# Optimization experiments

Measured on AMD Instinct MI355X. Metric: run time of the kernel, lower is better.

## Reference

```python
import jax, jax.numpy as jnp
import numpy as np

EMBED = 1024
HEADS = 16
HEAD_DIM = EMBED // HEADS
WIN = 256  # attention_window w; band width = 2w+1


def setup_inputs() -> dict:
    key = jax.random.key(0)
    ks = jax.random.split(key, 10)
    b, s, e = 2, 4096, EMBED
    scale = 1.0 / np.sqrt(e)
    inp = {"x": jax.random.normal(ks[0], (b, s, e), jnp.float32)}
    for i, (wn, bn) in enumerate([("Wq", "bq"), ("Wk", "bk"), ("Wv", "bv"), ("Wo", "bo")]):
        inp[wn] = jax.random.normal(ks[1 + i], (e, e), jnp.float32) * scale
        inp[bn] = jax.random.normal(ks[5 + i], (e,), jnp.float32) * 0.01
    return inp


def _rope_headaxis(x):
    # Replicates RotaryEmbedding applied to [b, s, h, d]: the original indexes
    # x.shape[2] (== num_heads here), so phase varies over the HEAD axis.
    h, d = x.shape[2], x.shape[3]
    inv = 1.0 / (10000.0 ** (jnp.arange(0, d, 2, dtype=jnp.float32) / d))
    freqs = jnp.arange(h, dtype=jnp.float32)[:, None] * inv[None, :]
    emb = jnp.concatenate([freqs, freqs], axis=-1)  # [h, d]
    cos = jnp.cos(emb)[None, None]  # [1,1,h,d]
    sin = jnp.sin(emb)[None, None]
    x2 = jnp.stack([-x[..., 1::2], x[..., 0::2]], axis=-1).reshape(x.shape)
    return x * cos + x2 * sin


def reference(x, Wq, bq, Wk, bk, Wv, bv, Wo, bo):
    b, s, e = x.shape
    h, d, w = HEADS, HEAD_DIM, WIN
    q = (x @ Wq.T + bq).reshape(b, s, h, d)
    k = (x @ Wk.T + bk).reshape(b, s, h, d)
    v = (x @ Wv.T + bv).reshape(b, s, h, d)
    q = _rope_headaxis(q) / jnp.sqrt(jnp.float32(d))
    k = _rope_headaxis(k)

    # Band (sliding-window) attention: query chunk c of size w attends to key
    # chunks c-1, c, c+1 (3w keys); relative-position + boundary masking makes
    # this identical to the original sliding_chunks band of width 2w+1.
    nc = s // w
    qc = q.reshape(b, nc, w, h, d)
    pad = [(0, 0), (w, w), (0, 0), (0, 0)]
    kp = jnp.pad(k, pad)
    vp = jnp.pad(v, pad)
    idx = jnp.arange(nc)[:, None] * w + jnp.arange(3 * w)[None, :]  # [nc, 3w]
    k3 = kp[:, idx]  # [b, nc, 3w, h, d]
    v3 = vp[:, idx]
    scores = jnp.einsum('bcxhd,bcyhd->bhcxy', qc, k3)  # [b,h,nc,w,3w]

    c = jnp.arange(nc)[:, None, None]
    xq = jnp.arange(w)[None, :, None]
    y = jnp.arange(3 * w)[None, None, :]
    kpos = c * w + y - w  # absolute key position
    valid = (y >= xq) & (y <= xq + 2 * w) & (kpos >= 0) & (kpos < s)
    scores = jnp.where(valid[None, None], scores, -jnp.inf)

    probs = jax.nn.softmax(scores, axis=-1)  # fp32 softmax, as in original
    ctx = jnp.einsum('bhcxy,bcyhd->bcxhd', probs, v3).reshape(b, s, e)
    return ctx @ Wo.T + bo
```

## Files before the change

### kernel.cpp

```cpp
#include <hip/hip_runtime.h>


typedef _Float16 half8 __attribute__((ext_vector_type(8)));
typedef _Float16 half4v __attribute__((ext_vector_type(4)));
typedef float floatx4 __attribute__((ext_vector_type(4)));

typedef __attribute__((address_space(3))) unsigned int lds_u32;
typedef const __attribute__((address_space(1))) unsigned int glb_u32;

__device__ __forceinline__ void async_copy16(const void* g, void* l) {
  __builtin_amdgcn_global_load_lds((glb_u32*)g, (lds_u32*)l, 16, 0, 0);
}

__global__ __launch_bounds__(256) void convert_kernel(
    const float* __restrict__ x, const float* __restrict__ wq,
    const float* __restrict__ wk, const float* __restrict__ wv,
    const float* __restrict__ wo, _Float16* __restrict__ dst) {
  const int e0 = (blockIdx.x * 256 + threadIdx.x) * 4;
  const float* src; int off;
  if      (e0 <  8388608) { src = x;  off = e0; }
  else if (e0 <  9437184) { src = wq; off = e0 -  8388608; }
  else if (e0 < 10485760) { src = wk; off = e0 -  9437184; }
  else if (e0 < 11534336) { src = wv; off = e0 - 10485760; }
  else                    { src = wo; off = e0 - 11534336; }
  const float4 f = *(const float4*)(src + off);
  half4v h;
  h[0] = (_Float16)f.x; h[1] = (_Float16)f.y;
  h[2] = (_Float16)f.z; h[3] = (_Float16)f.w;
  *(half4v*)(dst + e0) = h;
}

__global__ __launch_bounds__(256, 2) void gemm_qkv_kernel(
    const _Float16* __restrict__ A, const _Float16* __restrict__ w0,
    const _Float16* __restrict__ w1, const _Float16* __restrict__ w2,
    const float* __restrict__ b0, const float* __restrict__ b1,
    const float* __restrict__ b2, _Float16* __restrict__ o0,
    _Float16* __restrict__ o1, _Float16* __restrict__ o2) {
  __shared__ _Float16 smem[17408];
  _Float16* As = smem;
  _Float16* Bs = smem + 8192;

  const int tid = threadIdx.x;
  const int w = tid >> 6, lane = tid & 63;
  const int l4 = lane & 15, quad = lane >> 4;
  const int wm = w & 1, wn = w >> 1;

  const int bid = blockIdx.x;
  const int xcd = bid & 7, li = bid >> 3;
  const int z = li >> 6, r_ = li & 63;
  const int n_l = r_ >> 3, m_l = r_ & 7;
  const int m0 = (xcd * 8 + m_l) * 128;
  const int n0 = n_l * 128;

  const _Float16* B; const float* bias; _Float16* out;
  if (z == 0)      { B = w0; bias = b0; out = o0; }
  else if (z == 1) { B = w1; bias = b1; out = o1; }
  else             { B = w2; bias = b2; out = o2; }
  const bool dorope = z < 2;
  const float scl = (z == 0) ? 0.18033688f : 1.0f;

  const floatx4 zero = {0.f, 0.f, 0.f, 0.f};
  floatx4 acc[4][4];
#pragma unroll
  for (int i = 0; i < 4; ++i)
#pragma unroll
    for (int j = 0; j < 4; ++j) acc[i][j] = zero;

  for (int kt = 0; kt < 16; ++kt) {
    const int k0 = kt * 64;
#pragma unroll
    for (int i = 0; i < 4; ++i) {
      const int p = i * 256 + tid;
      const int r = p >> 3;
      const int c = (p & 7) ^ (r & 7);
      async_copy16(A + (m0 + r) * 1024 + k0 + c * 8, As + (i * 256 + w * 64) * 8);
      async_copy16(B + (n0 + r) * 1024 + k0 + c * 8, Bs + (i * 256 + w * 64) * 8);
    }
    __syncthreads();
#pragma unroll
    for (int ks = 0; ks < 2; ++ks) {
      half8 af[4], bf[4];
#pragma unroll
      for (int mt = 0; mt < 4; ++mt)
        af[mt] = *(const half8*)(As + (wm * 64 + mt * 16 + l4) * 64 +
                                 (((ks * 4 + quad) ^ (l4 & 7)) * 8));
#pragma unroll
      for (int nt = 0; nt < 4; ++nt)
        bf[nt] = *(const half8*)(Bs + (wn * 64 + nt * 16 + l4) * 64 +
                                 (((ks * 4 + quad) ^ (l4 & 7)) * 8));
#pragma unroll
      for (int mt = 0; mt < 4; ++mt)
#pragma unroll
        for (int nt = 0; nt < 4; ++nt)
          acc[mt][nt] = __builtin_amdgcn_mfma_f32_16x16x32_f16(af[mt], bf[nt], acc[mt][nt], 0, 0, 0);
    }
    __syncthreads();
  }

  _Float16* tile = smem;
#pragma unroll
  for (int nt = 0; nt < 4; ++nt) {
    const int n = n0 + wn * 64 + nt * 16 + l4;
    const float bval = bias[n];
    const int hh = n >> 6;
    float c_ = 1.f, ss = 0.f;
    if (dorope) {
      const float freq = __expf((float)(n & 31) * -0.28782314f);
      float s_;
      __sincosf((float)hh * freq, &s_, &c_);
      ss = (n & 1) ? s_ : -s_;
    }
#pragma unroll
    for (int mt = 0; mt < 4; ++mt)
#pragma unroll
      for (int r = 0; r < 4; ++r) {
        float val = acc[mt][nt][r] + bval;
        const float prt = __shfl_xor(val, 1);
        if (dorope) val = (val * c_ + prt * ss) * scl;
        tile[(wm * 64 + mt * 16 + quad * 4 + r) * 132 + wn * 64 + nt * 16 + l4] = (_Float16)val;
      }
  }
  __syncthreads();
#pragma unroll
  for (int j = 0; j < 8; ++j) {
    const int idx = j * 256 + tid;
    const int row = idx >> 4, cb = idx & 15;
    const int n = n0 + cb * 8;
    const int hh = n >> 6, dd = n & 63;
    const int m = m0 + row, bb = m >> 12, s = m & 4095;
    const half8 vals = *(const half8*)(tile + row * 132 + cb * 8);
    *(half8*)(out + ((bb * 16 + hh) * 4096 + s) * 64 + dd) = vals;
  }
}

__global__ __launch_bounds__(256, 2) void gemm_out_kernel(
    const _Float16* __restrict__ A, const _Float16* __restrict__ B,
    const float* __restrict__ bias, float* __restrict__ out) {
  __shared__ _Float16 smem[16384];
  _Float16* As = smem;
  _Float16* Bs = smem + 8192;

  const int tid = threadIdx.x;
  const int w = tid >> 6, lane = tid & 63;
  const int l4 = lane & 15, quad = lane >> 4;
  const int wm = w & 1, wn = w >> 1;

  const int bid = blockIdx.x;
  const int xcd = bid & 7, li = bid >> 3;
  const int n_l = li >> 3, m_l = li & 7;
  const int m0 = (xcd * 8 + m_l) * 128;
  const int n0 = n_l * 128;

  const floatx4 zero = {0.f, 0.f, 0.f, 0.f};
  floatx4 acc[4][4];
#pragma unroll
  for (int i = 0; i < 4; ++i)
#pragma unroll
    for (int j = 0; j < 4; ++j) acc[i][j] = zero;

  for (int kt = 0; kt < 16; ++kt) {
    const int k0 = kt * 64;
#pragma unroll
    for (int i = 0; i < 4; ++i) {
      const int p = i * 256 + tid;
      const int r = p >> 3;
      const int c = (p & 7) ^ (r & 7);
      async_copy16(A + (m0 + r) * 1024 + k0 + c * 8, As + (i * 256 + w * 64) * 8);
      async_copy16(B + (n0 + r) * 1024 + k0 + c * 8, Bs + (i * 256 + w * 64) * 8);
    }
    __syncthreads();
#pragma unroll
    for (int ks = 0; ks < 2; ++ks) {
      half8 af[4], bf[4];
#pragma unroll
      for (int mt = 0; mt < 4; ++mt)
        af[mt] = *(const half8*)(As + (wm * 64 + mt * 16 + l4) * 64 +
                                 (((ks * 4 + quad) ^ (l4 & 7)) * 8));
#pragma unroll
      for (int nt = 0; nt < 4; ++nt)
        bf[nt] = *(const half8*)(Bs + (wn * 64 + nt * 16 + l4) * 64 +
                                 (((ks * 4 + quad) ^ (l4 & 7)) * 8));
#pragma unroll
      for (int mt = 0; mt < 4; ++mt)
#pragma unroll
        for (int nt = 0; nt < 4; ++nt)
          acc[mt][nt] = __builtin_amdgcn_mfma_f32_16x16x32_f16(af[mt], bf[nt], acc[mt][nt], 0, 0, 0);
    }
    __syncthreads();
  }

#pragma unroll
  for (int nt = 0; nt < 4; ++nt) {
    const int n = n0 + wn * 64 + nt * 16 + l4;
    const float bval = bias[n];
#pragma unroll
    for (int mt = 0; mt < 4; ++mt)
#pragma unroll
      for (int r = 0; r < 4; ++r) {
        const int m = m0 + wm * 64 + mt * 16 + quad * 4 + r;
        out[m * 1024 + n] = acc[mt][nt][r] + bval;
      }
  }
}

__global__ __launch_bounds__(256) void transpose_v(const _Float16* __restrict__ v,
                                                   _Float16* __restrict__ vt) {
  __shared__ _Float16 tile[64 * 70];
  const int t = threadIdx.x;
  const int bh = blockIdx.y, s0 = blockIdx.x * 64;
  const _Float16* src = v + (bh * 4096 + s0) * 64;
#pragma unroll
  for (int i = 0; i < 2; ++i) {
    const int c = i * 256 + t;
    const int row = c >> 3, cb = c & 7;
    const half8 d = *(const half8*)(src + row * 64 + cb * 8);
#pragma unroll
    for (int u = 0; u < 8; ++u) tile[(cb * 8 + u) * 70 + row] = d[u];
  }
  __syncthreads();
  _Float16* dst = vt + bh * 262144 + s0;
#pragma unroll
  for (int i = 0; i < 2; ++i) {
    const int c = i * 256 + t;
    const int dd = c >> 3, scb = c & 7;
    half8 d;
#pragma unroll
    for (int u = 0; u < 8; ++u) d[u] = tile[dd * 70 + scb * 8 + u];
    *(half8*)(dst + dd * 4096 + scb * 8) = d;
  }
}

__global__ __launch_bounds__(256, 2) void attn_kernel(
    const _Float16* __restrict__ qg, const _Float16* __restrict__ kg,
    const _Float16* __restrict__ vtg, _Float16* __restrict__ ctx) {
  __shared__ _Float16 Ks[128 * 64];
  __shared__ _Float16 Vs[64 * 128];

  const int tid = threadIdx.x;
  const int w = tid >> 6, lane = tid & 63;
  const int l4 = lane & 15, quad = lane >> 4;
  const int q0 = blockIdx.x * 128;
  const int bh = blockIdx.y;
  const _Float16* qbh = qg + bh * 262144;
  const _Float16* kbh = kg + bh * 262144;
  const _Float16* vbh = vtg + bh * 262144;

  half8 qf[2][2];
#pragma unroll
  for (int nt = 0; nt < 2; ++nt)
#pragma unroll
    for (int ks = 0; ks < 2; ++ks)
      qf[nt][ks] = *(const half8*)(qbh + (q0 + w * 32 + nt * 16 + l4) * 64 + ks * 32 + quad * 8);

  const floatx4 zero = {0.f, 0.f, 0.f, 0.f};
  floatx4 OT[4][2];
  float m_st[2], l_st[2];
#pragma unroll
  for (int md = 0; md < 4; ++md)
#pragma unroll
    for (int nt = 0; nt < 2; ++nt) OT[md][nt] = zero;
#pragma unroll
  for (int nt = 0; nt < 2; ++nt) { m_st[nt] = -1e30f; l_st[nt] = 0.f; }

  for (int t = 0; t < 5; ++t) {
    const int kv0 = q0 + (t - 2) * 128;
    if (kv0 < 0 || kv0 >= 4096) continue;

#pragma unroll
    for (int i = 0; i < 4; ++i) {
      const int p = i * 256 + tid;
      const int rk = p >> 3, ck = (p & 7) ^ (rk & 7);
      async_copy16(kbh + (kv0 + rk) * 64 + ck * 8, Ks + (i * 256 + w * 64) * 8);
      const int rv = p >> 4, cv = (p & 15) ^ (rv & 7);
      async_copy16(vbh + rv * 4096 + kv0 + cv * 8, Vs + (i * 256 + w * 64) * 8);
    }
    __syncthreads();

    const bool edge = (t == 0 || t == 4);
#pragma unroll
    for (int hf = 0; hf < 2; ++hf) {
      const int kb = hf * 64;

      floatx4 ST[4][2];
#pragma unroll
      for (int m = 0; m < 4; ++m)
#pragma unroll
        for (int nt = 0; nt < 2; ++nt) ST[m][nt] = zero;
#pragma unroll
      for (int ks = 0; ks < 2; ++ks)
#pragma unroll
        for (int m = 0; m < 4; ++m) {
          const half8 kf = *(const half8*)(Ks + (kb + m * 16 + l4) * 64 +
                                           ((ks * 4 + quad) ^ (l4 & 7)) * 8);
#pragma unroll
          for (int nt = 0; nt < 2; ++nt)
            ST[m][nt] = __builtin_amdgcn_mfma_f32_16x16x32_f16(kf, qf[nt][ks], ST[m][nt], 0, 0, 0);
        }

      if (edge) {
#pragma unroll
        for (int m = 0; m < 4; ++m)
#pragma unroll
          for (int r = 0; r < 4; ++r) {
            const int key = kv0 + kb + m * 16 + quad * 4 + r;
#pragma unroll
            for (int nt = 0; nt < 2; ++nt) {
              const int d = key - (q0 + w * 32 + nt * 16 + l4);
              if (d < -256 || d > 256) ST[m][nt][r] = -1e30f;
            }
          }
      }

#pragma unroll
      for (int nt = 0; nt < 2; ++nt) {
        float mx = -1e30f;
#pragma unroll
        for (int m = 0; m < 4; ++m)
#pragma unroll
          for (int r = 0; r < 4; ++r) mx = fmaxf(mx, ST[m][nt][r]);
        mx = fmaxf(mx, __shfl_xor(mx, 16));
        mx = fmaxf(mx, __shfl_xor(mx, 32));
        const float mnew = fmaxf(m_st[nt], mx);
        const float alpha = exp2f(m_st[nt] - mnew);
        m_st[nt] = mnew;
        float rs = 0.f;
#pragma unroll
        for (int m = 0; m < 4; ++m)
#pragma unroll
          for (int r = 0; r < 4; ++r) {
            const float pv = exp2f(ST[m][nt][r] - mnew);
            ST[m][nt][r] = pv;
            rs += pv;
          }
        rs += __shfl_xor(rs, 16);
        rs += __shfl_xor(rs, 32);
        l_st[nt] = l_st[nt] * alpha + rs;
#pragma unroll
        for (int md = 0; md < 4; ++md)
#pragma unroll
          for (int r = 0; r < 4; ++r) OT[md][nt][r] *= alpha;
      }

#pragma unroll
      for (int m = 0; m < 4; ++m) {
        half4v pb[2];
#pragma unroll
        for (int nt = 0; nt < 2; ++nt) {
          const auto lo = __builtin_amdgcn_cvt_pkrtz(ST[m][nt][0], ST[m][nt][1]);
          const auto hi = __builtin_amdgcn_cvt_pkrtz(ST[m][nt][2], ST[m][nt][3]);
          pb[nt][0] = (_Float16)lo[0]; pb[nt][1] = (_Float16)lo[1];
          pb[nt][2] = (_Float16)hi[0]; pb[nt][3] = (_Float16)hi[1];
        }
#pragma unroll
        for (int md = 0; md < 4; ++md) {
          const half4v vf = *(const half4v*)(Vs + (md * 16 + l4) * 128 +
                                             (((hf * 8 + m * 2 + (quad >> 1)) ^ (l4 & 7)) * 8 +
                                              (quad & 1) * 4));
#pragma unroll
          for (int nt = 0; nt < 2; ++nt)
            OT[md][nt] = __builtin_amdgcn_mfma_f32_16x16x16f16(vf, pb[nt], OT[md][nt], 0, 0, 0);
        }
      }
    }
    __syncthreads();
  }

  const int b = bh >> 4, hh = bh & 15;
#pragma unroll
  for (int nt = 0; nt < 2; ++nt) {
    const float inv_l = 1.f / l_st[nt];
    const int s = q0 + w * 32 + nt * 16 + l4;
#pragma unroll
    for (int md = 0; md < 4; ++md) {
      half4v o;
#pragma unroll
      for (int r = 0; r < 4; ++r) o[r] = (_Float16)(OT[md][nt][r] * inv_l);
      *(half4v*)(ctx + (b * 4096 + s) * 1024 + hh * 64 + md * 16 + quad * 4) = o;
    }
  }
}

extern "C" void kernel_launch(void* const* d_in, const int* in_sizes, int n_in,
                              void* d_out, int out_size, void* d_ws, size_t ws_size,
                              hipStream_t stream) {
  const float* x  = (const float*)d_in[0];
  const float* Wq = (const float*)d_in[1];
  const float* bq = (const float*)d_in[2];
  const float* Wk = (const float*)d_in[3];
  const float* bk = (const float*)d_in[4];
  const float* Wv = (const float*)d_in[5];
  const float* bv = (const float*)d_in[6];
  const float* Wo = (const float*)d_in[7];
  const float* bo = (const float*)d_in[8];

  _Float16* ws   = (_Float16*)d_ws;
  _Float16* xh   = ws;
  _Float16* wqh  = ws + 8388608;
  _Float16* wkh  = ws + 9437184;
  _Float16* wvh  = ws + 10485760;
  _Float16* woh  = ws + 11534336;
  _Float16* qh   = ws + 12582912;
  _Float16* kh   = ws + 20971520;
  _Float16* vh   = ws + 29360128;
  _Float16* vth  = ws + 37748736;
  _Float16* ctxh = xh;

  convert_kernel<<<12288, 256, 0, stream>>>(x, Wq, Wk, Wv, Wo, ws);
  gemm_qkv_kernel<<<1536, 256, 0, stream>>>(xh, wqh, wkh, wvh,
                                            bq, bk, bv, qh, kh, vh);
  transpose_v<<<dim3(64, 32), 256, 0, stream>>>(vh, vth);
  attn_kernel<<<dim3(32, 32), 256, 0, stream>>>(qh, kh, vth, ctxh);
  gemm_out_kernel<<<512, 256, 0, stream>>>(ctxh, woh, bo, (float*)d_out);
}
```

Before: 256.6 us.

## Fuse V transpose into QKV GEMM epilogue and raise occupancy bounds

The QKV GEMM epilogue now writes the V projection directly in transposed [d, s] layout by staging through LDS transposed, removing the separate transpose_v kernel and its extra global read/write pass. Launch bounds for the GEMM and attention kernels are raised from 2 to 4 blocks per CU to raise occupancy. The occupancy hint tightens the register budget and may cause spills, and the transposed LDS writes may add bank conflicts.

```diff
diff --git a/kernel.cpp b/kernel.cpp
--- a/kernel.cpp
+++ b/kernel.cpp
@@ -30,7 +30,7 @@
   *(half4v*)(dst + e0) = h;
 }
 
-__global__ __launch_bounds__(256, 2) void gemm_qkv_kernel(
+__global__ __launch_bounds__(256, 4) void gemm_qkv_kernel(
     const _Float16* __restrict__ A, const _Float16* __restrict__ w0,
     const _Float16* __restrict__ w1, const _Float16* __restrict__ w2,
     const float* __restrict__ b0, const float* __restrict__ b1,
@@ -117,23 +117,37 @@
         float val = acc[mt][nt][r] + bval;
         const float prt = __shfl_xor(val, 1);
         if (dorope) val = (val * c_ + prt * ss) * scl;
-        tile[(wm * 64 + mt * 16 + quad * 4 + r) * 132 + wn * 64 + nt * 16 + l4] = (_Float16)val;
+        const int ml = wm * 64 + mt * 16 + quad * 4 + r;
+        const int nl = wn * 64 + nt * 16 + l4;
+        if (z == 2) tile[nl * 132 + ml] = (_Float16)val;
+        else        tile[ml * 132 + nl] = (_Float16)val;
       }
   }
   __syncthreads();
-#pragma unroll
-  for (int j = 0; j < 8; ++j) {
-    const int idx = j * 256 + tid;
-    const int row = idx >> 4, cb = idx & 15;
-    const int n = n0 + cb * 8;
-    const int hh = n >> 6, dd = n & 63;
-    const int m = m0 + row, bb = m >> 12, s = m & 4095;
-    const half8 vals = *(const half8*)(tile + row * 132 + cb * 8);
-    *(half8*)(out + ((bb * 16 + hh) * 4096 + s) * 64 + dd) = vals;
-  }
-}
-
-__global__ __launch_bounds__(256, 2) void gemm_out_kernel(
+  if (z == 2) {
+#pragma unroll
+    for (int j = 0; j < 8; ++j) {
+      const int idx = j * 256 + tid;
+      const int row = idx >> 4, cb = idx & 15;
+      const int n = n0 + row, hh = n >> 6, dd = n & 63;
+      const int m = m0 + cb * 8, bb = m >> 12, s = m & 4095;
+      const half8 vals = *(const half8*)(tile + row * 132 + cb * 8);
+      *(half8*)(out + (bb * 16 + hh) * 262144 + dd * 4096 + s) = vals;
+    }
+  } else {
+#pragma unroll
+    for (int j = 0; j < 8; ++j) {
+      const int idx = j * 256 + tid;
+      const int row = idx >> 4, cb = idx & 15;
+      const int n = n0 + cb * 8, hh = n >> 6, dd = n & 63;
+      const int m = m0 + row, bb = m >> 12, s = m & 4095;
+      const half8 vals = *(const half8*)(tile + row * 132 + cb * 8);
+      *(half8*)(out + ((bb * 16 + hh) * 4096 + s) * 64 + dd) = vals;
+    }
+  }
+}
+
+__global__ __launch_bounds__(256, 4) void gemm_out_kernel(
     const _Float16* __restrict__ A, const _Float16* __restrict__ B,
     const float* __restrict__ bias, float* __restrict__ out) {
   __shared__ _Float16 smem[16384];
@@ -203,34 +217,7 @@
   }
 }
 
-__global__ __launch_bounds__(256) void transpose_v(const _Float16* __restrict__ v,
-                                                   _Float16* __restrict__ vt) {
-  __shared__ _Float16 tile[64 * 70];
-  const int t = threadIdx.x;
-  const int bh = blockIdx.y, s0 = blockIdx.x * 64;
-  const _Float16* src = v + (bh * 4096 + s0) * 64;
-#pragma unroll
-  for (int i = 0; i < 2; ++i) {
-    const int c = i * 256 + t;
-    const int row = c >> 3, cb = c & 7;
-    const half8 d = *(const half8*)(src + row * 64 + cb * 8);
-#pragma unroll
-    for (int u = 0; u < 8; ++u) tile[(cb * 8 + u) * 70 + row] = d[u];
-  }
-  __syncthreads();
-  _Float16* dst = vt + bh * 262144 + s0;
-#pragma unroll
-  for (int i = 0; i < 2; ++i) {
-    const int c = i * 256 + t;
-    const int dd = c >> 3, scb = c & 7;
-    half8 d;
-#pragma unroll
-    for (int u = 0; u < 8; ++u) d[u] = tile[dd * 70 + scb * 8 + u];
-    *(half8*)(dst + dd * 4096 + scb * 8) = d;
-  }
-}
-
-__global__ __launch_bounds__(256, 2) void attn_kernel(
+__global__ __launch_bounds__(256, 4) void attn_kernel(
     const _Float16* __restrict__ qg, const _Float16* __restrict__ kg,
     const _Float16* __restrict__ vtg, _Float16* __restrict__ ctx) {
   __shared__ _Float16 Ks[128 * 64];
@@ -401,14 +388,12 @@
   _Float16* woh  = ws + 11534336;
   _Float16* qh   = ws + 12582912;
   _Float16* kh   = ws + 20971520;
-  _Float16* vh   = ws + 29360128;
-  _Float16* vth  = ws + 37748736;
+  _Float16* vth  = ws + 29360128;
   _Float16* ctxh = xh;
 
   convert_kernel<<<12288, 256, 0, stream>>>(x, Wq, Wk, Wv, Wo, ws);
   gemm_qkv_kernel<<<1536, 256, 0, stream>>>(xh, wqh, wkh, wvh,
-                                            bq, bk, bv, qh, kh, vh);
-  transpose_v<<<dim3(64, 32), 256, 0, stream>>>(vh, vth);
+                                            bq, bk, bv, qh, kh, vth);
   attn_kernel<<<dim3(32, 32), 256, 0, stream>>>(qh, kh, vth, ctxh);
   gemm_out_kernel<<<512, 256, 0, stream>>>(ctxh, woh, bo, (float*)d_out);
 }
```

After: 271.9 us. 6.0% more time.
